# Optimization experiments

Measured on AMD Instinct MI355X. Metric: run time of the kernel, lower is better.

## Reference

```python
import jax, jax.numpy as jnp
import numpy as np

N_USERS = 100000
N_ITEMS = 50000
N_NODES = N_USERS + N_ITEMS
D = 64          # embedding_size / d_model
L = 2           # n_layers (GCN layers and transformer layers)
H = 8           # nhead
FF = 2048       # TransformerEncoderLayer default dim_feedforward
E_RAND = 1600000
B = 4096
EPS = 1e-5


def setup_inputs() -> dict:
    key = jax.random.key(0)
    ks = jax.random.split(key, 24)
    s = 0.05
    users = jax.random.randint(ks[0], (B,), 0, N_USERS)
    items = jax.random.randint(ks[1], (B,), 0, N_ITEMS)
    src = jax.random.randint(ks[2], (E_RAND,), 0, N_NODES)
    dst = jax.random.randint(ks[3], (E_RAND,), 0, N_NODES)
    loops = jnp.arange(N_NODES)  # ensure degree >= 1 everywhere (real graphs have no isolated rows)
    edge_index = jnp.stack([jnp.concatenate([src, loops]), jnp.concatenate([dst, loops])])
    f32 = jnp.float32
    return {
        "users": users,
        "items": items,
        "edge_index": edge_index,
        "user_table": jax.random.normal(ks[4], (N_USERS, D), f32) * s,
        "item_table": jax.random.normal(ks[5], (N_ITEMS, D), f32) * s,
        "gl_W": jax.random.normal(ks[6], (L, D, D), f32) * s,
        "gl_b": jax.random.normal(ks[7], (L, D), f32) * s,
        "corr_W": jax.random.normal(ks[8], (D, D), f32) * s,
        "corr_b": jax.random.normal(ks[9], (D,), f32) * s,
        "qkv_W": jax.random.normal(ks[10], (L, D, 3 * D), f32) * s,
        "qkv_b": jax.random.normal(ks[11], (L, 3 * D), f32) * s,
        "out_W": jax.random.normal(ks[12], (L, D, D), f32) * s,
        "out_b": jax.random.normal(ks[13], (L, D), f32) * s,
        "ff1_W": jax.random.normal(ks[14], (L, D, FF), f32) * s,
        "ff1_b": jax.random.normal(ks[15], (L, FF), f32) * s,
        "ff2_W": jax.random.normal(ks[16], (L, FF, D), f32) * s,
        "ff2_b": jax.random.normal(ks[17], (L, D), f32) * s,
        "ln1_g": jnp.ones((L, D), f32),
        "ln1_b": jnp.zeros((L, D), f32),
        "ln2_g": jnp.ones((L, D), f32),
        "ln2_b": jnp.zeros((L, D), f32),
    }


def _layer_norm(x, g, b):
    m = jnp.mean(x, axis=-1, keepdims=True)
    v = jnp.mean(jnp.square(x - m), axis=-1, keepdims=True)
    return (x - m) * jax.lax.rsqrt(v + EPS) * g + b


def _transformer(x, qkv_W, qkv_b, out_W, out_b, ff1_W, ff1_b, ff2_W, ff2_b,
                 ln1_g, ln1_b, ln2_g, ln2_b):
    # x: [N, D]; original passes x.unsqueeze(0) with batch_first=False -> seq_len=1,
    # batch=N. Softmax over a single key is identity, so MHA(x) == out_proj(V(x)).
    for l in range(L):
        v = x @ qkv_W[l][:, 2 * D:] + qkv_b[l][2 * D:]          # [N, D] value projection
        attn = v @ out_W[l] + out_b[l]
        x = _layer_norm(x + attn, ln1_g[l], ln1_b[l])            # post-LN (PyTorch default)
        ffn = jax.nn.relu(x @ ff1_W[l] + ff1_b[l]) @ ff2_W[l] + ff2_b[l]
        x = _layer_norm(x + ffn, ln2_g[l], ln2_b[l])
    return x


def reference(users, items, edge_index, user_table, item_table, gl_W, gl_b,
              corr_W, corr_b, qkv_W, qkv_b, out_W, out_b, ff1_W, ff1_b,
              ff2_W, ff2_b, ln1_g, ln1_b, ln2_g, ln2_b):
    row, col = edge_index[0], edge_index[1]
    # degree-normalized scatter-add GCN propagation (GraphLayer.message)
    deg = jax.ops.segment_sum(jnp.ones(row.shape, user_table.dtype), row, num_segments=N_NODES)
    dis = deg ** -0.5
    norm = dis[row] * dis[col]                                   # [E]
    x = jnp.concatenate([user_table, item_table], axis=0)        # [N_NODES, D]
    for l in range(L):
        h = x @ gl_W[l] + gl_b[l]
        msg = norm[:, None] * h[row]                             # gather + edge norm
        x = jax.ops.segment_sum(msg, col, num_segments=N_NODES)  # scatter-add aggr
    user_g, item_g = x[:N_USERS], x[N_USERS:]
    # CrossModalCorrection: one shared Linear on both
    user_c = user_g @ corr_W + corr_b
    item_c = item_g @ corr_W + corr_b
    tf = lambda z: _transformer(z, qkv_W, qkv_b, out_W, out_b, ff1_W, ff1_b,
                                ff2_W, ff2_b, ln1_g, ln1_b, ln2_g, ln2_b)
    user_final = tf(user_c)
    item_final = tf(item_c)
    return jnp.sum(user_final[users] * item_final[items], axis=1)  # [B]
```

## Files before the change

kernel.cpp:

```cpp
#include <hip/hip_runtime.h>
#include <math.h>

#define NU 100000
#define NI 50000
#define NN 150000
#define NNP 150528
#define SCNB 147
#define LNEPS 1e-5f

typedef short bfx8 __attribute__((ext_vector_type(8)));
typedef float f32x4 __attribute__((ext_vector_type(4)));
#define MFMA16(a, b, c) __builtin_amdgcn_mfma_f32_16x16x32_bf16(a, b, c, 0, 0, 0)

__device__ __forceinline__ unsigned short f2bf(float f) {
    unsigned u = __float_as_uint(f);
    unsigned r = u + 0x7FFFu + ((u >> 16) & 1u);
    return (unsigned short)(r >> 16);
}

__global__ __launch_bounds__(256) void k_markS(const int* __restrict__ users,
                                               const int* __restrict__ items,
                                               unsigned* __restrict__ bS, int nb) {
    int t = blockIdx.x * 256 + threadIdx.x;
    if (t < 2 * nb) {
        int node = (t < nb) ? users[t] : (NU + items[t - nb]);
        atomicOr(&bS[node >> 5], 1u << (node & 31));
    }
}

__global__ __launch_bounds__(256) void k_pre1(const int* __restrict__ row,
                                              const int* __restrict__ col,
                                              const unsigned* __restrict__ bS,
                                              int* __restrict__ deg,
                                              unsigned* __restrict__ bR, int E) {
    int e = blockIdx.x * 256 + threadIdx.x;
    if (e >= E) return;
    int r = row[e];
    atomicAdd(&deg[r], 1);
    int c = col[e];
    if ((bS[c >> 5] >> (c & 31)) & 1u) atomicOr(&bR[r >> 5], 1u << (r & 31));
}

__global__ __launch_bounds__(256) void k_dis(const int* __restrict__ deg,
                                             float* __restrict__ dis) {
    int i = blockIdx.x * 256 + threadIdx.x;
    if (i < NN) dis[i] = rsqrtf((float)deg[i]);
}

__global__ __launch_bounds__(256) void k_cnt(const int* __restrict__ col,
                                             const unsigned* __restrict__ bR,
                                             int* __restrict__ cnt, int E) {
    int e = blockIdx.x * 256 + threadIdx.x;
    if (e >= E) return;
    int c = col[e];
    if ((bR[c >> 5] >> (c & 31)) & 1u) atomicAdd(&cnt[c], 1);
}

__global__ __launch_bounds__(256) void k_scan1(const int* __restrict__ cnt,
                                               int* __restrict__ bsum) {
    __shared__ int sh[256];
    int b = blockIdx.x, t = threadIdx.x;
    int4 v = ((const int4*)cnt)[b * 256 + t];
    sh[t] = v.x + v.y + v.z + v.w;
    __syncthreads();
    for (int off = 128; off >= 1; off >>= 1) {
        if (t < off) sh[t] += sh[t + off];
        __syncthreads();
    }
    if (t == 0) bsum[b] = sh[0];
}

__global__ __launch_bounds__(256) void k_scan2(int* __restrict__ bsum, int nblk) {
    __shared__ int sh[256];
    int t = threadIdx.x;
    int v = (t < nblk) ? bsum[t] : 0;
    sh[t] = v;
    __syncthreads();
    for (int off = 1; off < 256; off <<= 1) {
        int add = (t >= off) ? sh[t - off] : 0;
        __syncthreads();
        sh[t] += add;
        __syncthreads();
    }
    if (t < nblk) bsum[t] = sh[t] - v;
}

__global__ __launch_bounds__(256) void k_scan3(const int* __restrict__ cnt,
                                               const int* __restrict__ bsum,
                                               int* __restrict__ start) {
    __shared__ int sh[257];
    int b = blockIdx.x, t = threadIdx.x;
    int4 v = ((const int4*)cnt)[b * 256 + t];
    int s = v.x + v.y + v.z + v.w;
    sh[t + 1] = s;
    if (t == 0) sh[0] = 0;
    __syncthreads();
    for (int off = 1; off < 256; off <<= 1) {
        int add = sh[t + 1] + ((t + 1 > off) ? sh[t + 1 - off] : 0);
        __syncthreads();
        sh[t + 1] = add;
        __syncthreads();
    }
    int base = bsum[b] + sh[t];
    int i0 = b * 1024 + t * 4;
    start[i0 + 0] = base;  base += v.x;
    start[i0 + 1] = base;  base += v.y;
    start[i0 + 2] = base;  base += v.z;
    start[i0 + 3] = base;
    if (b == SCNB - 1 && t == 255) start[NNP] = base + v.w;
}

__global__ __launch_bounds__(256) void k_place(const int* __restrict__ row,
                                               const int* __restrict__ col,
                                               const unsigned* __restrict__ bR,
                                               const float* __restrict__ dis,
                                               const int* __restrict__ start,
                                               int* __restrict__ cur,
                                               int2* __restrict__ el, int E) {
    int e = blockIdx.x * 256 + threadIdx.x;
    if (e >= E) return;
    int c = col[e];
    if (!((bR[c >> 5] >> (c & 31)) & 1u)) return;
    int r = row[e];
    float nv = dis[r] * dis[c];
    int pos = atomicAdd(&cur[c], 1);
    el[start[c] + pos] = make_int2(r, __float_as_int(nv));
}

__global__ __launch_bounds__(256) void k_gather1(const int2* __restrict__ el,
                                                 const int* __restrict__ start,
                                                 const float* __restrict__ ut,
                                                 const float* __restrict__ itb,
                                                 float* __restrict__ g1,
                                                 float* __restrict__ sdeg) {
    int wid = (blockIdx.x * 256 + threadIdx.x) >> 6;
    int j = threadIdx.x & 63;
    if (wid >= NN) return;
    int s = start[wid], e = start[wid + 1];
    if (s == e) return;
    float acc0 = 0.f, acc1 = 0.f, sn = 0.f;
    int i = s;
    for (; i + 1 < e; i += 2) {
        int2 e0 = el[i], e1 = el[i + 1];
        float n0 = __int_as_float(e0.y), n1 = __int_as_float(e1.y);
        const float* s0 = (e0.x < NU) ? ut + (size_t)e0.x * 64
                                      : itb + (size_t)(e0.x - NU) * 64;
        const float* s1 = (e1.x < NU) ? ut + (size_t)e1.x * 64
                                      : itb + (size_t)(e1.x - NU) * 64;
        acc0 = fmaf(n0, s0[j], acc0);
        acc1 = fmaf(n1, s1[j], acc1);
        sn += n0 + n1;
    }
    if (i < e) {
        int2 e0 = el[i];
        float n0 = __int_as_float(e0.y);
        const float* s0 = (e0.x < NU) ? ut + (size_t)e0.x * 64
                                      : itb + (size_t)(e0.x - NU) * 64;
        acc0 = fmaf(n0, s0[j], acc0);
        sn += n0;
    }
    g1[(size_t)wid * 64 + j] = acc0 + acc1;
    if (j == 0) sdeg[wid] = sn;
}

__global__ __launch_bounds__(256) void k_gather2(const int2* __restrict__ el,
                                                 const int* __restrict__ start,
                                                 const float* __restrict__ g1,
                                                 const float* __restrict__ sdeg,
                                                 const unsigned* __restrict__ bS,
                                                 float* __restrict__ gg,
                                                 float* __restrict__ s2) {
    int wid = (blockIdx.x * 256 + threadIdx.x) >> 6;
    int j = threadIdx.x & 63;
    if (wid >= NN) return;
    if (!((bS[wid >> 5] >> (wid & 31)) & 1u)) return;
    int s = start[wid], e = start[wid + 1];
    float acc0 = 0.f, acc1 = 0.f, sa = 0.f;
    int i = s;
    for (; i + 1 < e; i += 2) {
        int2 e0 = el[i], e1 = el[i + 1];
        float n0 = __int_as_float(e0.y), n1 = __int_as_float(e1.y);
        acc0 = fmaf(n0, g1[(size_t)e0.x * 64 + j], acc0);
        acc1 = fmaf(n1, g1[(size_t)e1.x * 64 + j], acc1);
        sa = fmaf(n0, sdeg[e0.x], sa);
        sa = fmaf(n1, sdeg[e1.x], sa);
    }
    if (i < e) {
        int2 e0 = el[i];
        float n0 = __int_as_float(e0.y);
        acc0 = fmaf(n0, g1[(size_t)e0.x * 64 + j], acc0);
        sa = fmaf(n0, sdeg[e0.x], sa);
    }
    gg[(size_t)wid * 64 + j] = acc0 + acc1;
    if (j == 0) s2[wid] = sa;
}

__global__ __launch_bounds__(256) void k_fuse(const float* __restrict__ qkvW,
                                              const float* __restrict__ qkvB,
                                              const float* __restrict__ outW,
                                              const float* __restrict__ outB,
                                              float* __restrict__ Wva,
                                              float* __restrict__ bva) {
    int l = blockIdx.x;
    __shared__ float wo[4096];
    int tid = threadIdx.x, j = tid & 63, kq = tid >> 6;
    for (int i = tid; i < 4096; i += 256) wo[i] = outW[l * 4096 + i];
    __syncthreads();
    for (int kk = 0; kk < 16; ++kk) {
        int k = kq * 16 + kk;
        float acc = 0.f;
        for (int m = 0; m < 64; ++m)
            acc = fmaf(qkvW[(size_t)l * 64 * 192 + k * 192 + 128 + m],
                       wo[m * 64 + j], acc);
        Wva[l * 4096 + k * 64 + j] = acc;
    }
    if (tid < 64) {
        float acc = outB[l * 64 + j];
        for (int m = 0; m < 64; ++m)
            acc = fmaf(qkvB[l * 192 + 128 + m], wo[m * 64 + j], acc);
        bva[l * 64 + j] = acc;
    }
}

__global__ __launch_bounds__(256) void k_fuse2(const float* __restrict__ glW,
                                               const float* __restrict__ glB,
                                               const float* __restrict__ corrW,
                                               const float* __restrict__ corrB,
                                               float* __restrict__ Wff,
                                               float* __restrict__ bff) {
    __shared__ float A[4096];
    __shared__ float B[4096];
    __shared__ float T[4096];
    __shared__ float vec[64];
    int tid = threadIdx.x, j = tid & 63, kq = tid >> 6;
    for (int i = tid; i < 4096; i += 256) { A[i] = glW[4096 + i]; B[i] = corrW[i]; }
    __syncthreads();
    for (int kk = 0; kk < 16; ++kk) {
        int k = kq * 16 + kk;
        float acc = 0.f;
        for (int m = 0; m < 64; ++m) acc = fmaf(glW[k * 64 + m], A[m * 64 + j], acc);
        T[k * 64 + j] = acc;
    }
    if (tid < 64) {
        float v = 0.f;
        for (int m = 0; m < 64; ++m) v = fmaf(glB[m], A[m * 64 + tid], v);
        vec[tid] = v;
    }
    __syncthreads();
    for (int kk = 0; kk < 16; ++kk) {
        int k = kq * 16 + kk;
        float acc = 0.f;
        for (int m = 0; m < 64; ++m) acc = fmaf(T[k * 64 + m], B[m * 64 + j], acc);
        Wff[k * 64 + j] = acc;
    }
    if (kq == 0) {
        float a = 0.f;
        for (int m = 0; m < 64; ++m) a = fmaf(vec[m], B[m * 64 + j], a);
        bff[j] = a;
    } else if (kq == 1) {
        float a = 0.f;
        for (int m = 0; m < 64; ++m) a = fmaf(glB[64 + m], B[m * 64 + j], a);
        bff[64 + j] = a;
    } else if (kq == 2) {
        bff[128 + j] = corrB[j];
    }
}

__global__ __launch_bounds__(256) void k_wprep(const float* __restrict__ ff1W,
                                               const float* __restrict__ ff2W,
                                               unsigned short* __restrict__ Wt1,
                                               unsigned short* __restrict__ Wt2) {
    __shared__ float sh[64][65];
    int b = blockIdx.x;
    int l = b >> 6, rem = b & 63;
    int mat = rem >> 5, tile = rem & 31;
    const float* src; unsigned short* dst; int C, R, r0, c0;
    if (mat == 0) { src = ff1W + (size_t)l * 64 * 2048; dst = Wt1 + (size_t)l * 2048 * 64;
                    R = 64; C = 2048; r0 = 0; c0 = tile * 64; }
    else          { src = ff2W + (size_t)l * 2048 * 64; dst = Wt2 + (size_t)l * 64 * 2048;
                    R = 2048; C = 64; r0 = tile * 64; c0 = 0; }
    int tid = threadIdx.x;
    for (int it = 0; it < 16; ++it) {
        int idx = it * 256 + tid;
        int lr = idx >> 6, lc = idx & 63;
        sh[lr][lc] = src[(size_t)(r0 + lr) * C + (c0 + lc)];
    }
    __syncthreads();
    for (int it = 0; it < 16; ++it) {
        int idx = it * 256 + tid;
        int lc = idx >> 6, lr = idx & 63;
        dst[(size_t)(c0 + lc) * R + (r0 + lr)] = f2bf(sh[lr][lc]);
    }
}

__global__ __launch_bounds__(256) void k_proj(const float* __restrict__ gg,
                                              const float* __restrict__ sdeg,
                                              const float* __restrict__ s2,
                                              const int* __restrict__ users,
                                              const int* __restrict__ items,
                                              const float* __restrict__ Wff,
                                              const float* __restrict__ bff,
                                              float* __restrict__ Cb, int nb) {
    __shared__ float Ws[4096];
    __shared__ float xsh[16][64];
    __shared__ float ssh[16][2];
    int tid = threadIdx.x, j = tid & 63, rq = tid >> 6;
    for (int i = tid; i < 4096; i += 256) Ws[i] = Wff[i];
    int r0 = blockIdx.x * 16;
    for (int i = tid; i < 1024; i += 256) {
        int b = r0 + (i >> 6);
        int node = (b < nb) ? users[b] : (NU + items[b - nb]);
        xsh[i >> 6][i & 63] = gg[(size_t)node * 64 + (i & 63)];
    }
    if (tid < 16) {
        int b = r0 + tid;
        int node = (b < nb) ? users[b] : (NU + items[b - nb]);
        ssh[tid][0] = s2[node];
        ssh[tid][1] = sdeg[node];
    }
    __syncthreads();
    float b1j = bff[j], b2j = bff[64 + j], cbj = bff[128 + j];
    float acc[4];
#pragma unroll
    for (int i = 0; i < 4; ++i) acc[i] = cbj;
    for (int k = 0; k < 64; ++k) {
        float w = Ws[k * 64 + j];
#pragma unroll
        for (int i = 0; i < 4; ++i) acc[i] = fmaf(xsh[rq + 4 * i][k], w, acc[i]);
    }
#pragma unroll
    for (int i = 0; i < 4; ++i) {
        int r = rq + 4 * i;
        Cb[(size_t)(r0 + r) * 64 + j] = acc[i] + ssh[r][0] * b1j + ssh[r][1] * b2j;
    }
}

__global__ __launch_bounds__(256) void k_attn(float* __restrict__ Cb,
                                              unsigned short* __restrict__ xb,
                                              const float* __restrict__ Wva,
                                              const float* __restrict__ bva,
                                              const float* __restrict__ g,
                                              const float* __restrict__ bt,
                                              int layer) {
    __shared__ float Ws[4096];
    __shared__ float xs[16][64];
    int tid = threadIdx.x, j = tid & 63, rq = tid >> 6;
    const float* wv = Wva + layer * 4096;
    for (int i = tid; i < 4096; i += 256) Ws[i] = wv[i];
    int row0 = blockIdx.x * 16;
    for (int i = tid; i < 1024; i += 256)
        xs[i >> 6][i & 63] = Cb[(size_t)(row0 + (i >> 6)) * 64 + (i & 63)];
    __syncthreads();
    float bv = bva[layer * 64 + j];
    float gg = g[layer * 64 + j], bb = bt[layer * 64 + j];
    float acc[4];
#pragma unroll
    for (int i = 0; i < 4; ++i) acc[i] = bv;
    for (int k = 0; k < 64; ++k) {
        float w = Ws[k * 64 + j];
#pragma unroll
        for (int i = 0; i < 4; ++i) acc[i] = fmaf(xs[rq * 4 + i][k], w, acc[i]);
    }
#pragma unroll
    for (int i = 0; i < 4; ++i) {
        int r = rq * 4 + i;
        float xv = xs[r][j] + acc[i];
        float s = xv;
#pragma unroll
        for (int o = 32; o >= 1; o >>= 1) s += __shfl_xor(s, o, 64);
        float m = s * (1.0f / 64.0f);
        float d = xv - m;
        float s2v = d * d;
#pragma unroll
        for (int o = 32; o >= 1; o >>= 1) s2v += __shfl_xor(s2v, o, 64);
        float xn = d * rsqrtf(s2v * (1.0f / 64.0f) + LNEPS) * gg + bb;
        Cb[(size_t)(row0 + r) * 64 + j] = xn;
        xb[(size_t)(row0 + r) * 64 + j] = f2bf(xn);
    }
}

__global__ __launch_bounds__(512) void k_ffnm(float* __restrict__ Cb,
                                              const unsigned short* __restrict__ xb,
                                              const unsigned short* __restrict__ Wt1,
                                              const unsigned short* __restrict__ Wt2,
                                              const float* __restrict__ ff1B,
                                              const float* __restrict__ ff2B,
                                              const float* __restrict__ g2,
                                              const float* __restrict__ b2t,
                                              int layer) {
    __shared__ short ts[32 * 128];
    __shared__ float ys[32 * 64];
    const unsigned short* w1 = Wt1 + (size_t)layer * 2048 * 64;
    const unsigned short* w2 = Wt2 + (size_t)layer * 64 * 2048;
    const float* b1 = ff1B + layer * 2048;
    int tid = threadIdx.x;
    int lane = tid & 63, wv = tid >> 6;
    int g = lane >> 4, r16 = lane & 15;
    int row0 = blockIdx.x * 32;
    int nt2 = wv & 3, mh = wv >> 2;

    bfx8 ax[2][2];
#pragma unroll
    for (int mt = 0; mt < 2; ++mt)
#pragma unroll
        for (int ks = 0; ks < 2; ++ks)
            ax[mt][ks] = *(const bfx8*)(xb + ((size_t)(row0 + 16 * mt + r16)) * 64
                                        + 32 * ks + 8 * g);

    f32x4 yfA = {0.f, 0.f, 0.f, 0.f}, yfB = {0.f, 0.f, 0.f, 0.f};

    for (int hc = 0; hc < 16; ++hc) {
        int h = hc * 128 + wv * 16 + r16;
        float b1v = b1[h];
        f32x4 tf0 = {b1v, b1v, b1v, b1v}, tf1 = tf0;
#pragma unroll
        for (int ks = 0; ks < 2; ++ks) {
            bfx8 bw = *(const bfx8*)(w1 + (size_t)h * 64 + 32 * ks + 8 * g);
            tf0 = MFMA16(ax[0][ks], bw, tf0);
            tf1 = MFMA16(ax[1][ks], bw, tf1);
        }
        int col = wv * 16 + r16;
#pragma unroll
        for (int r = 0; r < 4; ++r) {
            int rowA = 4 * g + r, rowB = 16 + 4 * g + r;
            int offA = (rowA * 256 + col * 2) ^ ((rowA & 7) << 4);
            int offB = (rowB * 256 + col * 2) ^ ((rowB & 7) << 4);
            *(short*)((char*)ts + offA) = (short)f2bf(fmaxf(tf0[r], 0.f));
            *(short*)((char*)ts + offB) = (short)f2bf(fmaxf(tf1[r], 0.f));
        }
        __syncthreads();
        int trow = 16 * mh + r16;
#pragma unroll
        for (int ks2 = 0; ks2 < 4; ++ks2) {
            int kl = 32 * ks2 + 8 * g;
            int off = (trow * 256 + kl * 2) ^ ((trow & 7) << 4);
            bfx8 ta = *(const bfx8*)((char*)ts + off);
            bfx8 bw2 = *(const bfx8*)(w2 + ((size_t)(16 * nt2 + r16)) * 2048
                                      + hc * 128 + kl);
            if (ks2 & 1) yfB = MFMA16(ta, bw2, yfB);
            else         yfA = MFMA16(ta, bw2, yfA);
        }
        __syncthreads();
    }
#pragma unroll
    for (int r = 0; r < 4; ++r)
        ys[(16 * mh + 4 * g + r) * 64 + 16 * nt2 + r16] = yfA[r] + yfB[r];
    __syncthreads();
    float b2 = ff2B[layer * 64 + lane];
    float gg = g2[layer * 64 + lane], bb = b2t[layer * 64 + lane];
#pragma unroll
    for (int i = 0; i < 4; ++i) {
        int r = wv * 4 + i;
        float xv = Cb[(size_t)(row0 + r) * 64 + lane] + ys[r * 64 + lane] + b2;
        float s = xv;
#pragma unroll
        for (int o = 32; o >= 1; o >>= 1) s += __shfl_xor(s, o, 64);
        float m = s * (1.0f / 64.0f);
        float d = xv - m;
        float s2v = d * d;
#pragma unroll
        for (int o = 32; o >= 1; o >>= 1) s2v += __shfl_xor(s2v, o, 64);
        float xn = d * rsqrtf(s2v * (1.0f / 64.0f) + LNEPS) * gg + bb;
        Cb[(size_t)(row0 + r) * 64 + lane] = xn;
    }
}

__global__ __launch_bounds__(256) void k_dot(const float* __restrict__ Cb,
                                             float* __restrict__ out, int nb) {
    int t = blockIdx.x * 256 + threadIdx.x;
    int b = t >> 4;
    if (b >= nb) return;
    int q = (t & 15) * 4;
    const float4 u = *reinterpret_cast<const float4*>(Cb + (size_t)b * 64 + q);
    const float4 v = *reinterpret_cast<const float4*>(Cb + (size_t)(nb + b) * 64 + q);
    float s = u.x * v.x + u.y * v.y + u.z * v.z + u.w * v.w;
#pragma unroll
    for (int o = 8; o >= 1; o >>= 1) s += __shfl_xor(s, o, 16);
    if ((t & 15) == 0) out[b] = s;
}

extern "C" void kernel_launch(void* const* d_in, const int* in_sizes, int n_in,
                              void* d_out, int out_size, void* d_ws, size_t ws_size,
                              hipStream_t stream) {
    const int* users = (const int*)d_in[0];
    const int* items = (const int*)d_in[1];
    const int* ei    = (const int*)d_in[2];
    const float* ut  = (const float*)d_in[3];
    const float* itb = (const float*)d_in[4];
    const float* glW = (const float*)d_in[5];
    const float* glB = (const float*)d_in[6];
    const float* corrW = (const float*)d_in[7];
    const float* corrB = (const float*)d_in[8];
    const float* qkvW = (const float*)d_in[9];
    const float* qkvB = (const float*)d_in[10];
    const float* outW = (const float*)d_in[11];
    const float* outB = (const float*)d_in[12];
    const float* ff1W = (const float*)d_in[13];
    const float* ff1B = (const float*)d_in[14];
    const float* ff2W = (const float*)d_in[15];
    const float* ff2B = (const float*)d_in[16];
    const float* ln1g = (const float*)d_in[17];
    const float* ln1b = (const float*)d_in[18];
    const float* ln2g = (const float*)d_in[19];
    const float* ln2b = (const float*)d_in[20];

    const int E  = in_sizes[2] / 2;
    const int nb = in_sizes[0];
    const int nrows = 2 * nb;
    const int* rowp = ei;
    const int* colp = ei + E;

    char* w = (char*)d_ws;
    size_t off = 0;
    auto alloc = [&](size_t bytes) {
        char* p = w + off;
        off += (bytes + 255) & ~(size_t)255;
        return p;
    };
    int*      deg   = (int*)alloc((size_t)NN * 4);
    float*    dis   = (float*)alloc((size_t)NN * 4);
    unsigned* bS    = (unsigned*)alloc(((NN + 31) / 32) * 4);
    unsigned* bR    = (unsigned*)alloc(((NN + 31) / 32) * 4);
    int*      cnt   = (int*)alloc((size_t)NNP * 4);
    int*      start = (int*)alloc((size_t)(NNP + 1) * 4);
    int*      cur   = (int*)alloc((size_t)NN * 4);
    int*      bsum  = (int*)alloc((size_t)SCNB * 4);
    int2*     el    = (int2*)alloc((size_t)E * 8);
    float*    bufA  = (float*)alloc((size_t)NN * 64 * 4);
    float*    bufB  = (float*)alloc((size_t)NN * 64 * 4);
    float*    sdeg  = (float*)alloc((size_t)NN * 4);
    float*    s2    = (float*)alloc((size_t)NN * 4);
    float*    cb    = (float*)alloc((size_t)nrows * 64 * 4);
    float*    Wva   = (float*)alloc(2 * 4096 * 4);
    float*    bva   = (float*)alloc(2 * 64 * 4);
    float*    Wff   = (float*)alloc(4096 * 4);
    float*    bff   = (float*)alloc(192 * 4);
    unsigned short* xbb = (unsigned short*)alloc((size_t)nrows * 64 * 2);
    unsigned short* Wt1 = (unsigned short*)alloc((size_t)2 * 2048 * 64 * 2);
    unsigned short* Wt2 = (unsigned short*)alloc((size_t)2 * 64 * 2048 * 2);
    float*    outp  = (float*)d_out;

    hipMemsetAsync(deg, 0, (size_t)NN * 4, stream);
    hipMemsetAsync(bS, 0, ((NN + 31) / 32) * 4, stream);
    hipMemsetAsync(bR, 0, ((NN + 31) / 32) * 4, stream);
    hipMemsetAsync(cnt, 0, (size_t)NNP * 4, stream);
    hipMemsetAsync(cur, 0, (size_t)NN * 4, stream);

    int eb = (E + 255) / 256;
    int nnb = (NN + 255) / 256;

    k_markS<<<(2 * nb + 255) / 256, 256, 0, stream>>>(users, items, bS, nb);
    k_pre1<<<eb, 256, 0, stream>>>(rowp, colp, bS, deg, bR, E);
    k_dis<<<nnb, 256, 0, stream>>>(deg, dis);
    k_cnt<<<eb, 256, 0, stream>>>(colp, bR, cnt, E);
    k_scan1<<<SCNB, 256, 0, stream>>>(cnt, bsum);
    k_scan2<<<1, 256, 0, stream>>>(bsum, SCNB);
    k_scan3<<<SCNB, 256, 0, stream>>>(cnt, bsum, start);
    k_place<<<eb, 256, 0, stream>>>(rowp, colp, bR, dis, start, cur, el, E);
    k_fuse<<<2, 256, 0, stream>>>(qkvW, qkvB, outW, outB, Wva, bva);
    k_fuse2<<<1, 256, 0, stream>>>(glW, glB, corrW, corrB, Wff, bff);
    k_wprep<<<128, 256, 0, stream>>>(ff1W, ff2W, Wt1, Wt2);

    int agb = (NN + 3) / 4;

    k_gather1<<<agb, 256, 0, stream>>>(el, start, ut, itb, bufA, sdeg);
    k_gather2<<<agb, 256, 0, stream>>>(el, start, bufA, sdeg, bS, bufB, s2);
    k_proj<<<(nrows + 15) / 16, 256, 0, stream>>>(bufB, sdeg, s2, users, items,
                                                  Wff, bff, cb, nb);

    for (int l = 0; l < 2; ++l) {
        k_attn<<<nrows / 16, 256, 0, stream>>>(cb, xbb, Wva, bva, ln1g, ln1b, l);
        k_ffnm<<<nrows / 32, 512, 0, stream>>>(cb, xbb, Wt1, Wt2, ff1B, ff2B,
                                               ln2g, ln2b, l);
    }
    k_dot<<<(nb * 16 + 255) / 256, 256, 0, stream>>>(cb, outp, nb);
}
```

Baseline: 507.4 us.

## Build full CSC index-only edge list, apply degree norm at gather, double-buffer FFN tiles

```diff
diff --git a/kernel.cpp b/kernel.cpp
--- a/kernel.cpp
+++ b/kernel.cpp
@@ -28,16 +28,18 @@
     }
 }
 
-__global__ __launch_bounds__(256) void k_pre1(const int* __restrict__ row,
+__global__ __launch_bounds__(256) void k_pre0(const int* __restrict__ row,
                                               const int* __restrict__ col,
                                               const unsigned* __restrict__ bS,
                                               int* __restrict__ deg,
+                                              int* __restrict__ cnt,
                                               unsigned* __restrict__ bR, int E) {
     int e = blockIdx.x * 256 + threadIdx.x;
     if (e >= E) return;
     int r = row[e];
+    int c = col[e];
     atomicAdd(&deg[r], 1);
-    int c = col[e];
+    atomicAdd(&cnt[c], 1);
     if ((bS[c >> 5] >> (c & 31)) & 1u) atomicOr(&bR[r >> 5], 1u << (r & 31));
 }
 
@@ -45,15 +47,6 @@
                                              float* __restrict__ dis) {
     int i = blockIdx.x * 256 + threadIdx.x;
     if (i < NN) dis[i] = rsqrtf((float)deg[i]);
-}
-
-__global__ __launch_bounds__(256) void k_cnt(const int* __restrict__ col,
-                                             const unsigned* __restrict__ bR,
-                                             int* __restrict__ cnt, int E) {
-    int e = blockIdx.x * 256 + threadIdx.x;
-    if (e >= E) return;
-    int c = col[e];
-    if ((bR[c >> 5] >> (c & 31)) & 1u) atomicAdd(&cnt[c], 1);
 }
 
 __global__ __launch_bounds__(256) void k_scan1(const int* __restrict__ cnt,
@@ -112,23 +105,20 @@
 
 __global__ __launch_bounds__(256) void k_place(const int* __restrict__ row,
                                                const int* __restrict__ col,
-                                               const unsigned* __restrict__ bR,
-                                               const float* __restrict__ dis,
                                                const int* __restrict__ start,
                                                int* __restrict__ cur,
-                                               int2* __restrict__ el, int E) {
+                                               int* __restrict__ el, int E) {
     int e = blockIdx.x * 256 + threadIdx.x;
     if (e >= E) return;
     int c = col[e];
-    if (!((bR[c >> 5] >> (c & 31)) & 1u)) return;
-    int r = row[e];
-    float nv = dis[r] * dis[c];
     int pos = atomicAdd(&cur[c], 1);
-    el[start[c] + pos] = make_int2(r, __float_as_int(nv));
-}
-
-__global__ __launch_bounds__(256) void k_gather1(const int2* __restrict__ el,
+    el[start[c] + pos] = row[e];
+}
+
+__global__ __launch_bounds__(256) void k_gather1(const int* __restrict__ el,
                                                  const int* __restrict__ start,
+                                                 const float* __restrict__ dis,
+                                                 const unsigned* __restrict__ filt,
                                                  const float* __restrict__ ut,
                                                  const float* __restrict__ itb,
                                                  float* __restrict__ g1,
@@ -136,38 +126,41 @@
     int wid = (blockIdx.x * 256 + threadIdx.x) >> 6;
     int j = threadIdx.x & 63;
     if (wid >= NN) return;
+    if (!((filt[wid >> 5] >> (wid & 31)) & 1u)) return;
     int s = start[wid], e = start[wid + 1];
-    if (s == e) return;
-    float acc0 = 0.f, acc1 = 0.f, sn = 0.f;
+    float a0 = 0.f, a1 = 0.f, a2 = 0.f, a3 = 0.f, sn = 0.f;
     int i = s;
-    for (; i + 1 < e; i += 2) {
-        int2 e0 = el[i], e1 = el[i + 1];
-        float n0 = __int_as_float(e0.y), n1 = __int_as_float(e1.y);
-        const float* s0 = (e0.x < NU) ? ut + (size_t)e0.x * 64
-                                      : itb + (size_t)(e0.x - NU) * 64;
-        const float* s1 = (e1.x < NU) ? ut + (size_t)e1.x * 64
-                                      : itb + (size_t)(e1.x - NU) * 64;
-        acc0 = fmaf(n0, s0[j], acc0);
-        acc1 = fmaf(n1, s1[j], acc1);
-        sn += n0 + n1;
-    }
-    if (i < e) {
-        int2 e0 = el[i];
-        float n0 = __int_as_float(e0.y);
-        const float* s0 = (e0.x < NU) ? ut + (size_t)e0.x * 64
-                                      : itb + (size_t)(e0.x - NU) * 64;
-        acc0 = fmaf(n0, s0[j], acc0);
-        sn += n0;
-    }
-    g1[(size_t)wid * 64 + j] = acc0 + acc1;
-    if (j == 0) sdeg[wid] = sn;
-}
-
-__global__ __launch_bounds__(256) void k_gather2(const int2* __restrict__ el,
+    for (; i + 3 < e; i += 4) {
+        int r0 = el[i], r1 = el[i + 1], r2 = el[i + 2], r3 = el[i + 3];
+        float d0 = dis[r0], d1 = dis[r1], d2 = dis[r2], d3 = dis[r3];
+        const float* p0 = (r0 < NU) ? ut + (size_t)r0 * 64 : itb + (size_t)(r0 - NU) * 64;
+        const float* p1 = (r1 < NU) ? ut + (size_t)r1 * 64 : itb + (size_t)(r1 - NU) * 64;
+        const float* p2 = (r2 < NU) ? ut + (size_t)r2 * 64 : itb + (size_t)(r2 - NU) * 64;
+        const float* p3 = (r3 < NU) ? ut + (size_t)r3 * 64 : itb + (size_t)(r3 - NU) * 64;
+        a0 = fmaf(d0, p0[j], a0);
+        a1 = fmaf(d1, p1[j], a1);
+        a2 = fmaf(d2, p2[j], a2);
+        a3 = fmaf(d3, p3[j], a3);
+        sn += (d0 + d1) + (d2 + d3);
+    }
+    for (; i < e; ++i) {
+        int r0 = el[i];
+        float d0 = dis[r0];
+        const float* p0 = (r0 < NU) ? ut + (size_t)r0 * 64 : itb + (size_t)(r0 - NU) * 64;
+        a0 = fmaf(d0, p0[j], a0);
+        sn += d0;
+    }
+    float dc = dis[wid];
+    g1[(size_t)wid * 64 + j] = dc * ((a0 + a1) + (a2 + a3));
+    if (j == 0) sdeg[wid] = dc * sn;
+}
+
+__global__ __launch_bounds__(256) void k_gather2(const int* __restrict__ el,
                                                  const int* __restrict__ start,
+                                                 const float* __restrict__ dis,
+                                                 const unsigned* __restrict__ bS,
                                                  const float* __restrict__ g1,
                                                  const float* __restrict__ sdeg,
-                                                 const unsigned* __restrict__ bS,
                                                  float* __restrict__ gg,
                                                  float* __restrict__ s2) {
     int wid = (blockIdx.x * 256 + threadIdx.x) >> 6;
@@ -175,24 +168,29 @@
     if (wid >= NN) return;
     if (!((bS[wid >> 5] >> (wid & 31)) & 1u)) return;
     int s = start[wid], e = start[wid + 1];
-    float acc0 = 0.f, acc1 = 0.f, sa = 0.f;
+    float a0 = 0.f, a1 = 0.f, a2 = 0.f, a3 = 0.f, sa = 0.f;
     int i = s;
-    for (; i + 1 < e; i += 2) {
-        int2 e0 = el[i], e1 = el[i + 1];
-        float n0 = __int_as_float(e0.y), n1 = __int_as_float(e1.y);
-        acc0 = fmaf(n0, g1[(size_t)e0.x * 64 + j], acc0);
-        acc1 = fmaf(n1, g1[(size_t)e1.x * 64 + j], acc1);
-        sa = fmaf(n0, sdeg[e0.x], sa);
-        sa = fmaf(n1, sdeg[e1.x], sa);
-    }
-    if (i < e) {
-        int2 e0 = el[i];
-        float n0 = __int_as_float(e0.y);
-        acc0 = fmaf(n0, g1[(size_t)e0.x * 64 + j], acc0);
-        sa = fmaf(n0, sdeg[e0.x], sa);
-    }
-    gg[(size_t)wid * 64 + j] = acc0 + acc1;
-    if (j == 0) s2[wid] = sa;
+    for (; i + 3 < e; i += 4) {
+        int r0 = el[i], r1 = el[i + 1], r2 = el[i + 2], r3 = el[i + 3];
+        float d0 = dis[r0], d1 = dis[r1], d2 = dis[r2], d3 = dis[r3];
+        a0 = fmaf(d0, g1[(size_t)r0 * 64 + j], a0);
+        a1 = fmaf(d1, g1[(size_t)r1 * 64 + j], a1);
+        a2 = fmaf(d2, g1[(size_t)r2 * 64 + j], a2);
+        a3 = fmaf(d3, g1[(size_t)r3 * 64 + j], a3);
+        sa = fmaf(d0, sdeg[r0], sa);
+        sa = fmaf(d1, sdeg[r1], sa);
+        sa = fmaf(d2, sdeg[r2], sa);
+        sa = fmaf(d3, sdeg[r3], sa);
+    }
+    for (; i < e; ++i) {
+        int r0 = el[i];
+        float d0 = dis[r0];
+        a0 = fmaf(d0, g1[(size_t)r0 * 64 + j], a0);
+        sa = fmaf(d0, sdeg[r0], sa);
+    }
+    float dc = dis[wid];
+    gg[(size_t)wid * 64 + j] = dc * ((a0 + a1) + (a2 + a3));
+    if (j == 0) s2[wid] = dc * sa;
 }
 
 __global__ __launch_bounds__(256) void k_fuse(const float* __restrict__ qkvW,
@@ -388,7 +386,7 @@
                                               const float* __restrict__ g2,
                                               const float* __restrict__ b2t,
                                               int layer) {
-    __shared__ short ts[32 * 128];
+    __shared__ short ts[2][32 * 128];
     __shared__ float ys[32 * 64];
     const unsigned short* w1 = Wt1 + (size_t)layer * 2048 * 64;
     const unsigned short* w2 = Wt2 + (size_t)layer * 64 * 2048;
@@ -408,38 +406,49 @@
                                         + 32 * ks + 8 * g);
 
     f32x4 yfA = {0.f, 0.f, 0.f, 0.f}, yfB = {0.f, 0.f, 0.f, 0.f};
-
-    for (int hc = 0; hc < 16; ++hc) {
-        int h = hc * 128 + wv * 16 + r16;
-        float b1v = b1[h];
-        f32x4 tf0 = {b1v, b1v, b1v, b1v}, tf1 = tf0;
-#pragma unroll
-        for (int ks = 0; ks < 2; ++ks) {
-            bfx8 bw = *(const bfx8*)(w1 + (size_t)h * 64 + 32 * ks + 8 * g);
-            tf0 = MFMA16(ax[0][ks], bw, tf0);
-            tf1 = MFMA16(ax[1][ks], bw, tf1);
+    int col = wv * 16 + r16;
+    int trow = 16 * mh + r16;
+
+    for (int hc2 = 0; hc2 < 8; ++hc2) {
+        bfx8 w2f[2][4];
+#pragma unroll
+        for (int sub = 0; sub < 2; ++sub)
+#pragma unroll
+            for (int ks2 = 0; ks2 < 4; ++ks2)
+                w2f[sub][ks2] = *(const bfx8*)(w2 + ((size_t)(16 * nt2 + r16)) * 2048
+                                               + (hc2 * 2 + sub) * 128
+                                               + 32 * ks2 + 8 * g);
+#pragma unroll
+        for (int sub = 0; sub < 2; ++sub) {
+            int h = (hc2 * 2 + sub) * 128 + wv * 16 + r16;
+            float b1v = b1[h];
+            f32x4 tf0 = {b1v, b1v, b1v, b1v}, tf1 = tf0;
+#pragma unroll
+            for (int ks = 0; ks < 2; ++ks) {
+                bfx8 bw = *(const bfx8*)(w1 + (size_t)h * 64 + 32 * ks + 8 * g);
+                tf0 = MFMA16(ax[0][ks], bw, tf0);
+                tf1 = MFMA16(ax[1][ks], bw, tf1);
+            }
+#pragma unroll
+            for (int r = 0; r < 4; ++r) {
+                int rowA = 4 * g + r, rowB = 16 + 4 * g + r;
+                int offA = (rowA * 256 + col * 2) ^ ((rowA & 7) << 4);
+                int offB = (rowB * 256 + col * 2) ^ ((rowB & 7) << 4);
+                *(short*)((char*)ts[sub] + offA) = (short)f2bf(fmaxf(tf0[r], 0.f));
+                *(short*)((char*)ts[sub] + offB) = (short)f2bf(fmaxf(tf1[r], 0.f));
+            }
         }
-        int col = wv * 16 + r16;
-#pragma unroll
-        for (int r = 0; r < 4; ++r) {
-            int rowA = 4 * g + r, rowB = 16 + 4 * g + r;
-            int offA = (rowA * 256 + col * 2) ^ ((rowA & 7) << 4);
-            int offB = (rowB * 256 + col * 2) ^ ((rowB & 7) << 4);
-            *(short*)((char*)ts + offA) = (short)f2bf(fmaxf(tf0[r], 0.f));
-            *(short*)((char*)ts + offB) = (short)f2bf(fmaxf(tf1[r], 0.f));
-        }
-        __syncthreads();
-        int trow = 16 * mh + r16;
-#pragma unroll
-        for (int ks2 = 0; ks2 < 4; ++ks2) {
-            int kl = 32 * ks2 + 8 * g;
-            int off = (trow * 256 + kl * 2) ^ ((trow & 7) << 4);
-            bfx8 ta = *(const bfx8*)((char*)ts + off);
-            bfx8 bw2 = *(const bfx8*)(w2 + ((size_t)(16 * nt2 + r16)) * 2048
-                                      + hc * 128 + kl);
-            if (ks2 & 1) yfB = MFMA16(ta, bw2, yfB);
-            else         yfA = MFMA16(ta, bw2, yfA);
-        }
+        __syncthreads();
+#pragma unroll
+        for (int sub = 0; sub < 2; ++sub)
+#pragma unroll
+            for (int ks2 = 0; ks2 < 4; ++ks2) {
+                int kl = 32 * ks2 + 8 * g;
+                int off2 = (trow * 256 + kl * 2) ^ ((trow & 7) << 4);
+                bfx8 ta = *(const bfx8*)((char*)ts[sub] + off2);
+                if (ks2 & 1) yfB = MFMA16(ta, w2f[sub][ks2], yfB);
+                else         yfA = MFMA16(ta, w2f[sub][ks2], yfA);
+            }
         __syncthreads();
     }
 #pragma unroll
@@ -525,7 +534,7 @@
     int*      start = (int*)alloc((size_t)(NNP + 1) * 4);
     int*      cur   = (int*)alloc((size_t)NN * 4);
     int*      bsum  = (int*)alloc((size_t)SCNB * 4);
-    int2*     el    = (int2*)alloc((size_t)E * 8);
+    int*      el    = (int*)alloc((size_t)E * 4);
     float*    bufA  = (float*)alloc((size_t)NN * 64 * 4);
     float*    bufB  = (float*)alloc((size_t)NN * 64 * 4);
     float*    sdeg  = (float*)alloc((size_t)NN * 4);
@@ -550,21 +559,20 @@
     int nnb = (NN + 255) / 256;
 
     k_markS<<<(2 * nb + 255) / 256, 256, 0, stream>>>(users, items, bS, nb);
-    k_pre1<<<eb, 256, 0, stream>>>(rowp, colp, bS, deg, bR, E);
+    k_pre0<<<eb, 256, 0, stream>>>(rowp, colp, bS, deg, cnt, bR, E);
     k_dis<<<nnb, 256, 0, stream>>>(deg, dis);
-    k_cnt<<<eb, 256, 0, stream>>>(colp, bR, cnt, E);
     k_scan1<<<SCNB, 256, 0, stream>>>(cnt, bsum);
     k_scan2<<<1, 256, 0, stream>>>(bsum, SCNB);
     k_scan3<<<SCNB, 256, 0, stream>>>(cnt, bsum, start);
-    k_place<<<eb, 256, 0, stream>>>(rowp, colp, bR, dis, start, cur, el, E);
+    k_place<<<eb, 256, 0, stream>>>(rowp, colp, start, cur, el, E);
     k_fuse<<<2, 256, 0, stream>>>(qkvW, qkvB, outW, outB, Wva, bva);
     k_fuse2<<<1, 256, 0, stream>>>(glW, glB, corrW, corrB, Wff, bff);
     k_wprep<<<128, 256, 0, stream>>>(ff1W, ff2W, Wt1, Wt2);
 
     int agb = (NN + 3) / 4;
 
-    k_gather1<<<agb, 256, 0, stream>>>(el, start, ut, itb, bufA, sdeg);
-    k_gather2<<<agb, 256, 0, stream>>>(el, start, bufA, sdeg, bS, bufB, s2);
+    k_gather1<<<agb, 256, 0, stream>>>(el, start, dis, bR, ut, itb, bufA, sdeg);
+    k_gather2<<<agb, 256, 0, stream>>>(el, start, dis, bS, bufA, sdeg, bufB, s2);
     k_proj<<<(nrows + 15) / 16, 256, 0, stream>>>(bufB, sdeg, s2, users, items,
                                                   Wff, bff, cb, nb);
 
```

Result: slower. 574.6 us (+13.2%).
